# Optimization experiments

Measured on AMD Instinct MI355X. Metric: run time of the kernel, lower is better.

## Reference

```python
import jax, jax.numpy as jnp
import numpy as np

D_MODEL, N_EXPERTS, TOP_K, D_FF = 1024, 8, 2, 4096
B, T = 2, 2048


def setup_inputs() -> dict:
    key = jax.random.key(0)
    k1, k2, k3, k4 = jax.random.split(key, 4)
    x = jax.random.normal(k1, (B, T, D_MODEL), dtype=jnp.float32)
    # kaiming-uniform-ish gate init
    bound = np.sqrt(6.0 / D_MODEL)
    gate_w = jax.random.uniform(k2, (D_MODEL, N_EXPERTS), dtype=jnp.float32, minval=-bound, maxval=bound)
    s1 = 1.0 / np.sqrt(D_MODEL)
    s2 = 1.0 / np.sqrt(D_FF)
    w1 = jax.random.normal(k3, (N_EXPERTS, D_MODEL, D_FF), dtype=jnp.float32) * s1
    w2 = jax.random.normal(k4, (N_EXPERTS, D_FF, D_MODEL), dtype=jnp.float32) * s2
    return {"x": x, "gate_w": gate_w, "w1": w1, "w2": w2}


def reference(x, gate_w, w1, w2):
    Bb, Tt, D = x.shape
    E = w1.shape[0]
    # --- router ---
    logits = jnp.einsum('btd,de->bte', x, gate_w)            # (B,T,E)
    top_v, top_i = jax.lax.top_k(logits, TOP_K)               # (B,T,K)
    weights = jax.nn.softmax(top_v, axis=-1)                  # (B,T,K)
    routing_probs = jax.nn.softmax(logits, axis=-1)           # (B,T,E)
    m = routing_probs.mean(axis=(0, 1))                       # (E,)
    aux_loss = (m * m).sum() * E
    # --- dispatch/combine via dense combine matrix ---
    N = Bb * Tt
    flat_x = x.reshape(N, D)
    idx = top_i.reshape(N, TOP_K)
    w = weights.reshape(N, TOP_K)
    # combine[n,e] = sum_k weights[n,k] * [idx[n,k]==e]
    combine = jnp.zeros((N, E), dtype=x.dtype).at[jnp.arange(N)[:, None], idx].add(w)
    # --- experts: Linear -> GELU(exact) -> Linear (HolographicExpert stand-in) ---
    h = jax.nn.gelu(jnp.einsum('nd,edf->enf', flat_x, w1), approximate=False)  # (E,N,ff)
    y = jnp.einsum('enf,efd->end', h, w2)                                       # (E,N,d)
    out = jnp.einsum('ne,end->nd', combine, y).reshape(Bb, Tt, D)
    return out, aux_loss
```

## Files before the change

### kernel.cpp

```cpp
#include <hip/hip_runtime.h>
#include <hip/hip_bf16.h>

#define DM   1024
#define NE   8
#define DFF  4096
#define NTOK 4096

typedef __attribute__((ext_vector_type(8))) short bf16x8;
typedef __attribute__((ext_vector_type(4))) float f32x4;

__device__ __forceinline__ short to_bf16(float f) {
  unsigned u = __float_as_uint(f);
  unsigned r = (u + 0x7fffu + ((u >> 16) & 1u)) >> 16;
  return (short)r;
}

__device__ __forceinline__ void gl16(const void* g, void* l) {
  __builtin_amdgcn_global_load_lds(
      (const __attribute__((address_space(1))) unsigned*)g,
      (__attribute__((address_space(3))) unsigned*)l, 16, 0, 0);
}

#define DSB do { __builtin_amdgcn_s_barrier(); __builtin_amdgcn_sched_barrier(0); } while (0)

__device__ __forceinline__ float fast_gelu(float v) {
  float x  = fabsf(v) * 0.70710678118f;
  float t  = __builtin_amdgcn_rcpf(fmaf(0.3275911f, x, 1.0f));
  float p  = t * fmaf(t, fmaf(t, fmaf(t, fmaf(t, 1.061405429f, -1.453152027f),
                                      1.421413741f), -0.284496736f), 0.254829592f);
  float ex = __expf(-x * x);
  float er = fmaf(-p, ex, 1.0f);
  er = (v < 0.f) ? -er : er;
  return 0.5f * v * (1.0f + er);
}

__global__ __launch_bounds__(256) void router_kernel(
    const float* __restrict__ x, const float* __restrict__ gw,
    int* __restrict__ cnt, float* __restrict__ psum,
    int* __restrict__ pairs, float* __restrict__ pairW)
{
  __shared__ float gws[DM * NE];
  __shared__ float part[3][64][NE];
  const int tid = threadIdx.x;
  for (int i = tid * 4; i < DM * NE; i += 256 * 4)
    *reinterpret_cast<float4*>(&gws[i]) = *reinterpret_cast<const float4*>(&gw[i]);
  __syncthreads();

  const int tok = tid & 63;
  const int q   = tid >> 6;
  const int n   = blockIdx.x * 64 + tok;
  float acc[NE];
#pragma unroll
  for (int e = 0; e < NE; ++e) acc[e] = 0.f;

  const float4* xr = reinterpret_cast<const float4*>(x + (size_t)n * DM + q * 256);
  for (int d4 = 0; d4 < 64; ++d4) {
    float4 v = xr[d4];
    const float* gp = &gws[(q * 256 + d4 * 4) * NE];
    float xv;
#pragma unroll
    for (int dd = 0; dd < 4; ++dd) {
      xv = (dd == 0) ? v.x : (dd == 1) ? v.y : (dd == 2) ? v.z : v.w;
#pragma unroll
      for (int e = 0; e < NE; ++e) acc[e] = fmaf(xv, gp[dd * NE + e], acc[e]);
    }
  }

  if (q) {
#pragma unroll
    for (int e = 0; e < NE; ++e) part[q - 1][tok][e] = acc[e];
  }
  __syncthreads();
  if (q == 0) {
#pragma unroll
    for (int e = 0; e < NE; ++e)
      acc[e] += part[0][tok][e] + part[1][tok][e] + part[2][tok][e];

    float mx = acc[0];
#pragma unroll
    for (int e = 1; e < NE; ++e) mx = fmaxf(mx, acc[e]);
    float p[NE], s = 0.f;
#pragma unroll
    for (int e = 0; e < NE; ++e) { p[e] = expf(acc[e] - mx); s += p[e]; }
    float inv = 1.f / s;
#pragma unroll
    for (int e = 0; e < NE; ++e) {
      float v = p[e] * inv;
#pragma unroll
      for (int o = 32; o > 0; o >>= 1) v += __shfl_xor(v, o);
      if (tok == 0) atomicAdd(&psum[e], v);
    }

    float v0 = -1e30f, v1 = -1e30f; int i0 = 0, i1 = 0;
#pragma unroll
    for (int e = 0; e < NE; ++e) {
      float l = acc[e];
      if (l > v0) { v1 = v0; i1 = i0; v0 = l; i0 = e; }
      else if (l > v1) { v1 = l; i1 = e; }
    }
    float e1 = expf(v1 - v0);
    float den = 1.f + e1;
    pairW[n * 2]     = 1.f / den;
    pairW[n * 2 + 1] = e1 / den;
    int p0 = atomicAdd(&cnt[i0], 1); pairs[i0 * NTOK + p0] = n * 2;
    int p1 = atomicAdd(&cnt[i1], 1); pairs[i1 * NTOK + p1] = n * 2 + 1;
  }
}

__global__ void finalize_kernel(const int* __restrict__ cnt, int* __restrict__ off,
                                const float* __restrict__ psum, float* __restrict__ aux)
{
  if (threadIdx.x == 0 && blockIdx.x == 0) {
    int o = 0;
    for (int e = 0; e < NE; ++e) { off[e] = o; o += cnt[e]; }
    off[NE] = o;
    float a = 0.f;
    for (int e = 0; e < NE; ++e) { float me = psum[e] * (1.f / NTOK); a += me * me; }
    aux[0] = a * (float)NE;
  }
}

__global__ __launch_bounds__(256) void convert_x_kernel(
    const float* __restrict__ x, short* __restrict__ xb)
{
  const int i = (blockIdx.x * 256 + threadIdx.x) * 8;
  float4 a = *reinterpret_cast<const float4*>(&x[i]);
  float4 b = *reinterpret_cast<const float4*>(&x[i + 4]);
  union { short s[8]; bf16x8 v; } p;
  p.s[0]=to_bf16(a.x); p.s[1]=to_bf16(a.y); p.s[2]=to_bf16(a.z); p.s[3]=to_bf16(a.w);
  p.s[4]=to_bf16(b.x); p.s[5]=to_bf16(b.y); p.s[6]=to_bf16(b.z); p.s[7]=to_bf16(b.w);
  *reinterpret_cast<bf16x8*>(&xb[i]) = p.v;
}

__global__ __launch_bounds__(256) void transpose_kernel(
    const float* __restrict__ w1, const float* __restrict__ w2,
    short* __restrict__ w1t, short* __restrict__ w2t)
{
  const int z = blockIdx.z;
  const float* src; short* dst; int R, C, rt, ct;
  if (z < 8) { src = w1 + (size_t)z * DM * DFF; dst = w1t + (size_t)z * DM * DFF;
               R = DM; C = DFF; ct = blockIdx.x; rt = blockIdx.y; }
  else       { src = w2 + (size_t)(z - 8) * DM * DFF; dst = w2t + (size_t)(z - 8) * DM * DFF;
               R = DFF; C = DM; ct = blockIdx.y; rt = blockIdx.x; }
  const int r0 = rt * 64, c0 = ct * 64;
  __shared__ float t[64][65];
  const int tid = threadIdx.x;
  {
    const int row = tid >> 4;
    const int col = (tid & 15) * 4;
#pragma unroll
    for (int it = 0; it < 4; ++it) {
      float4 v = *reinterpret_cast<const float4*>(&src[(size_t)(r0 + it * 16 + row) * C + c0 + col]);
      t[it * 16 + row][col]     = v.x;
      t[it * 16 + row][col + 1] = v.y;
      t[it * 16 + row][col + 2] = v.z;
      t[it * 16 + row][col + 3] = v.w;
    }
  }
  __syncthreads();
  {
    const int oc  = tid >> 3;
    const int orr = (tid & 7) * 8;
#pragma unroll
    for (int it = 0; it < 2; ++it) {
      union { short s[8]; bf16x8 v; } p;
#pragma unroll
      for (int j = 0; j < 8; ++j) p.s[j] = to_bf16(t[orr + j][it * 32 + oc]);
      *reinterpret_cast<bf16x8*>(&dst[(size_t)(c0 + it * 32 + oc) * R + r0 + orr]) = p.v;
    }
  }
}


#define GEMM_LOOP(NT)                                                              \
  f32x4 acc[4][4];                                                                 \
  _Pragma("unroll") for (int i = 0; i < 4; ++i)                                    \
    _Pragma("unroll") for (int j = 0; j < 4; ++j) acc[i][j] = (f32x4){0.f,0.f,0.f,0.f}; \
  STAGE(0, 0);                                                                     \
  STAGE(1, 32);                                                                    \
  {                                                                                \
    int cur = 0, stg = 2;                                                          \
    for (int t = 0; t < (NT); ++t) {                                               \
      if (t < (NT) - 1) { asm volatile("s_waitcnt vmcnt(4)" ::: "memory"); }       \
      else              { asm volatile("s_waitcnt vmcnt(0)" ::: "memory"); }       \
      DSB;                                                                         \
      if (t + 2 < (NT)) STAGE(stg, (t + 2) * 32);                                  \
      bf16x8 af[4], bfv[4];                                                        \
      _Pragma("unroll") for (int i = 0; i < 4; ++i)                                \
        af[i] = *reinterpret_cast<const bf16x8*>(&As[cur][ab + i * 512]);          \
      _Pragma("unroll") for (int j = 0; j < 4; ++j)                                \
        bfv[j] = *reinterpret_cast<const bf16x8*>(&Bs[cur][bb + j * 512]);         \
      _Pragma("unroll") for (int i = 0; i < 4; ++i)                                \
        _Pragma("unroll") for (int j = 0; j < 4; ++j)                              \
          acc[i][j] = __builtin_amdgcn_mfma_f32_16x16x32_bf16(af[i], bfv[j], acc[i][j], 0, 0, 0); \
      cur = (cur == 2) ? 0 : cur + 1;                                              \
      stg = (stg == 2) ? 0 : stg + 1;                                              \
    }                                                                              \
  }

__global__ __launch_bounds__(256) void gemm1_kernel(
    const short* __restrict__ xb, const short* __restrict__ w1t,
    const int* __restrict__ cnt, const int* __restrict__ off,
    const int* __restrict__ pairs, short* __restrict__ h)
{
  const int wg = (blockIdx.x & 7) * 1024 + (blockIdx.x >> 3);
  const int mt = wg & 31;
  const int ft = (wg >> 5) & 31;
  const int e  = wg >> 10;
  const int M  = cnt[e];
  const int m0 = mt * 128;
  if (m0 >= M) return;
  const int ff0  = ft * 128;
  const int base = off[e];

  __shared__ __attribute__((aligned(16))) short As[3][128 * 32];
  __shared__ __attribute__((aligned(16))) short Bs[3][128 * 32];

  const int tid  = threadIdx.x;
  const int lane = tid & 63;
  const int wv   = tid >> 6;
  const int wm   = wv >> 1;
  const int wn   = wv & 1;

  const short* gA[2]; const short* gB[2]; int ldo[2];
#pragma unroll
  for (int l = 0; l < 2; ++l) {
    const int n   = l * 256 + tid;
    const int p   = n >> 3;
    const int s   = n & 7;
    const int cip = s ^ (p & 7);
    const int row = p * 2 + (cip >> 2);
    const int kch = cip & 3;
    int gi = m0 + row; if (gi > M - 1) gi = M - 1;
    const int tok = pairs[e * NTOK + gi] >> 1;
    gA[l]  = xb + (size_t)tok * DM + kch * 8;
    gB[l]  = w1t + ((size_t)e * DFF + ff0 + row) * DM + kch * 8;
    ldo[l] = n * 8;
  }

#define STAGE(buf, k0) do { \
  gl16(gA[0] + (k0), &As[buf][ldo[0]]); \
  gl16(gA[1] + (k0), &As[buf][ldo[1]]); \
  gl16(gB[0] + (k0), &Bs[buf][ldo[0]]); \
  gl16(gB[1] + (k0), &Bs[buf][ldo[1]]); \
} while (0)

  const int lrw = lane & 15;
  const int sr  = ((((lane & 1) << 2) | (lane >> 4)) ^ ((lane & 15) >> 1)) * 8;
  const int ab  = (wm * 32 + (lrw >> 1)) * 64 + sr;
  const int bb  = (wn * 32 + (lrw >> 1)) * 64 + sr;

  GEMM_LOOP(32)
#undef STAGE

  const int erow0 = m0 + wm * 64 + (lane >> 4) * 4;
  const int ecol0 = ff0 + wn * 64 + (lane & 15);
#pragma unroll
  for (int i = 0; i < 4; ++i) {
#pragma unroll
    for (int r = 0; r < 4; ++r) {
      const int grow = erow0 + i * 16 + r;
      if (grow < M) {
        short* hp = h + (size_t)(base + grow) * DFF + ecol0;
#pragma unroll
        for (int j = 0; j < 4; ++j)
          hp[j * 16] = to_bf16(fast_gelu(acc[i][j][r]));
      }
    }
  }
}

__global__ __launch_bounds__(256) void gemm2_kernel(
    const short* __restrict__ h, const short* __restrict__ w2t,
    const int* __restrict__ cnt, const int* __restrict__ off,
    const int* __restrict__ pairs, const float* __restrict__ pairW,
    float* __restrict__ out)
{
  const int wg = (blockIdx.x & 7) * 256 + (blockIdx.x >> 3);
  const int dt = wg & 7;
  const int mt = (wg >> 3) & 31;
  const int e  = wg >> 8;
  const int M  = cnt[e];
  const int m0 = mt * 128;
  if (m0 >= M) return;
  const int d0   = dt * 128;
  const int base = off[e];

  __shared__ __attribute__((aligned(16))) short As[3][128 * 32];
  __shared__ __attribute__((aligned(16))) short Bs[3][128 * 32];

  const int tid  = threadIdx.x;
  const int lane = tid & 63;
  const int wv   = tid >> 6;
  const int wm   = wv >> 1;
  const int wn   = wv & 1;

  const short* gA[2]; const short* gB[2]; int ldo[2];
#pragma unroll
  for (int l = 0; l < 2; ++l) {
    const int n   = l * 256 + tid;
    const int p   = n >> 3;
    const int s   = n & 7;
    const int cip = s ^ (p & 7);
    const int row = p * 2 + (cip >> 2);
    const int kch = cip & 3;
    int gi = m0 + row; if (gi > M - 1) gi = M - 1;
    gA[l]  = h + (size_t)(base + gi) * DFF + kch * 8;
    gB[l]  = w2t + ((size_t)e * DM + d0 + row) * DFF + kch * 8;
    ldo[l] = n * 8;
  }

#define STAGE(buf, k0) do { \
  gl16(gA[0] + (k0), &As[buf][ldo[0]]); \
  gl16(gA[1] + (k0), &As[buf][ldo[1]]); \
  gl16(gB[0] + (k0), &Bs[buf][ldo[0]]); \
  gl16(gB[1] + (k0), &Bs[buf][ldo[1]]); \
} while (0)

  const int lrw = lane & 15;
  const int sr  = ((((lane & 1) << 2) | (lane >> 4)) ^ ((lane & 15) >> 1)) * 8;
  const int ab  = (wm * 32 + (lrw >> 1)) * 64 + sr;
  const int bb  = (wn * 32 + (lrw >> 1)) * 64 + sr;

  GEMM_LOOP(128)
#undef STAGE

  const int erow0 = m0 + wm * 64 + (lane >> 4) * 4;
  const int ecol0 = d0 + wn * 64 + (lane & 15);
#pragma unroll
  for (int i = 0; i < 4; ++i) {
#pragma unroll
    for (int r = 0; r < 4; ++r) {
      const int grow = erow0 + i * 16 + r;
      if (grow < M) {
        const int pr    = pairs[e * NTOK + grow];
        const float wgt = pairW[pr];
        const int tok   = pr >> 1;
#pragma unroll
        for (int j = 0; j < 4; ++j)
          atomicAdd(&out[(size_t)tok * DM + ecol0 + j * 16], wgt * acc[i][j][r]);
      }
    }
  }
}

extern "C" void kernel_launch(void* const* d_in, const int* in_sizes, int n_in,
                              void* d_out, int out_size, void* d_ws, size_t ws_size,
                              hipStream_t stream)
{
  const float* x  = (const float*)d_in[0];
  const float* gw = (const float*)d_in[1];
  const float* w1 = (const float*)d_in[2];
  const float* w2 = (const float*)d_in[3];
  float* outf = (float*)d_out;

  int*   cnt   = (int*)d_ws;
  int*   off   = cnt + 8;
  float* psum  = (float*)(cnt + 20);
  int*   pairs = (int*)((char*)d_ws + 512);
  float* pairW = (float*)((char*)d_ws + 512 + NE * NTOK * 4);
  short* xb    = (short*)((char*)d_ws + (size_t)(1)  * (1 << 20));
  short* w1t   = (short*)((char*)d_ws + (size_t)(16) * (1 << 20));
  short* w2t   = (short*)((char*)d_ws + (size_t)(80) * (1 << 20));
  short* h     = (short*)((char*)d_ws + (size_t)(144)* (1 << 20));

  hipMemsetAsync(d_ws, 0, 512, stream);
  hipMemsetAsync(d_out, 0, (size_t)out_size * sizeof(float), stream);

  router_kernel<<<NTOK / 64, 256, 0, stream>>>(x, gw, cnt, psum, pairs, pairW);
  finalize_kernel<<<1, 64, 0, stream>>>(cnt, off, psum, outf + (size_t)NTOK * DM);
  convert_x_kernel<<<NTOK * DM / (256 * 8), 256, 0, stream>>>(x, xb);
  transpose_kernel<<<dim3(64, 16, 16), 256, 0, stream>>>(w1, w2, w1t, w2t);
  gemm1_kernel<<<8192, 256, 0, stream>>>(xb, w1t, cnt, off, pairs, h);
  gemm2_kernel<<<2048, 256, 0, stream>>>(h, w2t, cnt, off, pairs, pairW, outf);
}
```

Before: 396.2 us.

## Fuse weight fp32-to-bf16 conversion and transpose into GEMM B-tile loads

```diff
diff --git a/kernel.cpp b/kernel.cpp
--- a/kernel.cpp
+++ b/kernel.cpp
@@ -132,74 +132,74 @@
   *reinterpret_cast<bf16x8*>(&xb[i]) = p.v;
 }
 
-__global__ __launch_bounds__(256) void transpose_kernel(
-    const float* __restrict__ w1, const float* __restrict__ w2,
-    short* __restrict__ w1t, short* __restrict__ w2t)
-{
-  const int z = blockIdx.z;
-  const float* src; short* dst; int R, C, rt, ct;
-  if (z < 8) { src = w1 + (size_t)z * DM * DFF; dst = w1t + (size_t)z * DM * DFF;
-               R = DM; C = DFF; ct = blockIdx.x; rt = blockIdx.y; }
-  else       { src = w2 + (size_t)(z - 8) * DM * DFF; dst = w2t + (size_t)(z - 8) * DM * DFF;
-               R = DFF; C = DM; ct = blockIdx.y; rt = blockIdx.x; }
-  const int r0 = rt * 64, c0 = ct * 64;
-  __shared__ float t[64][65];
-  const int tid = threadIdx.x;
-  {
-    const int row = tid >> 4;
-    const int col = (tid & 15) * 4;
-#pragma unroll
-    for (int it = 0; it < 4; ++it) {
-      float4 v = *reinterpret_cast<const float4*>(&src[(size_t)(r0 + it * 16 + row) * C + c0 + col]);
-      t[it * 16 + row][col]     = v.x;
-      t[it * 16 + row][col + 1] = v.y;
-      t[it * 16 + row][col + 2] = v.z;
-      t[it * 16 + row][col + 3] = v.w;
-    }
-  }
-  __syncthreads();
-  {
-    const int oc  = tid >> 3;
-    const int orr = (tid & 7) * 8;
-#pragma unroll
-    for (int it = 0; it < 2; ++it) {
-      union { short s[8]; bf16x8 v; } p;
-#pragma unroll
-      for (int j = 0; j < 8; ++j) p.s[j] = to_bf16(t[orr + j][it * 32 + oc]);
-      *reinterpret_cast<bf16x8*>(&dst[(size_t)(c0 + it * 32 + oc) * R + r0 + orr]) = p.v;
-    }
-  }
-}
-
-
-#define GEMM_LOOP(NT)                                                              \
+
+#define CVTW(buf, S) do {                                                          \
+    int4 _w0, _w1;                                                                 \
+    asm("v_cvt_pk_bf16_f32 %0, %1, %2" : "=v"(_w0.x) : "v"(S[0].x), "v"(S[1].x)); \
+    asm("v_cvt_pk_bf16_f32 %0, %1, %2" : "=v"(_w0.y) : "v"(S[2].x), "v"(S[3].x)); \
+    asm("v_cvt_pk_bf16_f32 %0, %1, %2" : "=v"(_w0.z) : "v"(S[4].x), "v"(S[5].x)); \
+    asm("v_cvt_pk_bf16_f32 %0, %1, %2" : "=v"(_w0.w) : "v"(S[6].x), "v"(S[7].x)); \
+    asm("v_cvt_pk_bf16_f32 %0, %1, %2" : "=v"(_w1.x) : "v"(S[0].y), "v"(S[1].y)); \
+    asm("v_cvt_pk_bf16_f32 %0, %1, %2" : "=v"(_w1.y) : "v"(S[2].y), "v"(S[3].y)); \
+    asm("v_cvt_pk_bf16_f32 %0, %1, %2" : "=v"(_w1.z) : "v"(S[4].y), "v"(S[5].y)); \
+    asm("v_cvt_pk_bf16_f32 %0, %1, %2" : "=v"(_w1.w) : "v"(S[6].y), "v"(S[7].y)); \
+    *reinterpret_cast<int4*>(&Bs[buf][wo0]) = _w0;                                 \
+    *reinterpret_cast<int4*>(&Bs[buf][wo1]) = _w1;                                 \
+  } while (0)
+
+#define LOADB(S, k0) do {                                                          \
+    const float* _p = gBp + (size_t)(k0) * KSTRIDE;                                \
+    _Pragma("unroll") for (int _j = 0; _j < 8; ++_j)                               \
+      S[_j] = *reinterpret_cast<const float2*>(_p + (size_t)_j * KSTRIDE);         \
+  } while (0)
+
+#define STAGEA(buf, k0) do {                                                       \
+    gl16(gA0 + (k0), &As[buf][ldo0]);                                              \
+    gl16(gA1 + (k0), &As[buf][ldo1]);                                              \
+  } while (0)
+
+#define GITER(t, NT, SC, SL) {                                                     \
+    const int cur = (t) & 1;                                                       \
+    if ((t) < (NT) - 1) { asm volatile("s_waitcnt vmcnt(8)" ::: "memory"); }       \
+    else                { asm volatile("s_waitcnt vmcnt(0)" ::: "memory"); }       \
+    DSB;                                                                           \
+    bf16x8 af[4], bfv[4];                                                          \
+    _Pragma("unroll") for (int _i = 0; _i < 4; ++_i)                               \
+      af[_i] = *reinterpret_cast<const bf16x8*>(&As[cur][ab + _i * 512]);          \
+    _Pragma("unroll") for (int _j = 0; _j < 4; ++_j)                               \
+      bfv[_j] = *reinterpret_cast<const bf16x8*>(&Bs[cur][bb + _j * 512]);         \
+    if ((t) + 1 < (NT)) {                                                          \
+      STAGEA(cur ^ 1, ((t) + 1) * 32);                                             \
+      CVTW(cur ^ 1, SC);                                                           \
+      __builtin_amdgcn_sched_barrier(0);                                           \
+    }                                                                              \
+    if ((t) + 2 < (NT)) LOADB(SL, ((t) + 2) * 32);                                 \
+    _Pragma("unroll") for (int _i = 0; _i < 4; ++_i)                               \
+      _Pragma("unroll") for (int _j = 0; _j < 4; ++_j)                             \
+        acc[_i][_j] = __builtin_amdgcn_mfma_f32_16x16x32_bf16(af[_i], bfv[_j], acc[_i][_j], 0, 0, 0); \
+    asm volatile("s_waitcnt lgkmcnt(0)" ::: "memory");                             \
+  }
+
+#define GEMM_PRO_LOOP(NT)                                                          \
   f32x4 acc[4][4];                                                                 \
   _Pragma("unroll") for (int i = 0; i < 4; ++i)                                    \
     _Pragma("unroll") for (int j = 0; j < 4; ++j) acc[i][j] = (f32x4){0.f,0.f,0.f,0.f}; \
-  STAGE(0, 0);                                                                     \
-  STAGE(1, 32);                                                                    \
-  {                                                                                \
-    int cur = 0, stg = 2;                                                          \
-    for (int t = 0; t < (NT); ++t) {                                               \
-      if (t < (NT) - 1) { asm volatile("s_waitcnt vmcnt(4)" ::: "memory"); }       \
-      else              { asm volatile("s_waitcnt vmcnt(0)" ::: "memory"); }       \
-      DSB;                                                                         \
-      if (t + 2 < (NT)) STAGE(stg, (t + 2) * 32);                                  \
-      bf16x8 af[4], bfv[4];                                                        \
-      _Pragma("unroll") for (int i = 0; i < 4; ++i)                                \
-        af[i] = *reinterpret_cast<const bf16x8*>(&As[cur][ab + i * 512]);          \
-      _Pragma("unroll") for (int j = 0; j < 4; ++j)                                \
-        bfv[j] = *reinterpret_cast<const bf16x8*>(&Bs[cur][bb + j * 512]);         \
-      _Pragma("unroll") for (int i = 0; i < 4; ++i)                                \
-        _Pragma("unroll") for (int j = 0; j < 4; ++j)                              \
-          acc[i][j] = __builtin_amdgcn_mfma_f32_16x16x32_bf16(af[i], bfv[j], acc[i][j], 0, 0, 0); \
-      cur = (cur == 2) ? 0 : cur + 1;                                              \
-      stg = (stg == 2) ? 0 : stg + 1;                                              \
-    }                                                                              \
+  float2 sA[8], sB[8];                                                             \
+  LOADB(sA, 0);                                                                    \
+  __builtin_amdgcn_sched_barrier(0);                                               \
+  STAGEA(0, 0);                                                                    \
+  __builtin_amdgcn_sched_barrier(0);                                               \
+  CVTW(0, sA);                                                                     \
+  __builtin_amdgcn_sched_barrier(0);                                               \
+  LOADB(sA, 32);                                                                   \
+  asm volatile("s_waitcnt lgkmcnt(0)" ::: "memory");                               \
+  for (int t = 0; t < (NT); t += 2) {                                              \
+    GITER(t, (NT), sA, sB)                                                         \
+    GITER(t + 1, (NT), sB, sA)                                                     \
   }
 
 __global__ __launch_bounds__(256) void gemm1_kernel(
-    const short* __restrict__ xb, const short* __restrict__ w1t,
+    const short* __restrict__ xb, const float* __restrict__ w1,
     const int* __restrict__ cnt, const int* __restrict__ off,
     const int* __restrict__ pairs, short* __restrict__ h)
 {
@@ -213,45 +213,40 @@
   const int ff0  = ft * 128;
   const int base = off[e];
 
-  __shared__ __attribute__((aligned(16))) short As[3][128 * 32];
-  __shared__ __attribute__((aligned(16))) short Bs[3][128 * 32];
+  __shared__ __attribute__((aligned(16))) short As[2][4096];
+  __shared__ __attribute__((aligned(16))) short Bs[2][4096];
 
   const int tid  = threadIdx.x;
   const int lane = tid & 63;
   const int wv   = tid >> 6;
-  const int wm   = wv >> 1;
-  const int wn   = wv & 1;
-
-  const short* gA[2]; const short* gB[2]; int ldo[2];
-#pragma unroll
-  for (int l = 0; l < 2; ++l) {
-    const int n   = l * 256 + tid;
-    const int p   = n >> 3;
-    const int s   = n & 7;
-    const int cip = s ^ (p & 7);
-    const int row = p * 2 + (cip >> 2);
-    const int kch = cip & 3;
+  const int wm   = wv >> 1, wn = wv & 1;
+
+  const short *gA0, *gA1; int ldo0, ldo1;
+  {
+    int n = tid, p = n >> 3, s = n & 7, cip = s ^ (p & 7);
+    int row = p * 2 + (cip >> 2), kch = cip & 3;
     int gi = m0 + row; if (gi > M - 1) gi = M - 1;
-    const int tok = pairs[e * NTOK + gi] >> 1;
-    gA[l]  = xb + (size_t)tok * DM + kch * 8;
-    gB[l]  = w1t + ((size_t)e * DFF + ff0 + row) * DM + kch * 8;
-    ldo[l] = n * 8;
-  }
-
-#define STAGE(buf, k0) do { \
-  gl16(gA[0] + (k0), &As[buf][ldo[0]]); \
-  gl16(gA[1] + (k0), &As[buf][ldo[1]]); \
-  gl16(gB[0] + (k0), &Bs[buf][ldo[0]]); \
-  gl16(gB[1] + (k0), &Bs[buf][ldo[1]]); \
-} while (0)
-
-  const int lrw = lane & 15;
-  const int sr  = ((((lane & 1) << 2) | (lane >> 4)) ^ ((lane & 15) >> 1)) * 8;
-  const int ab  = (wm * 32 + (lrw >> 1)) * 64 + sr;
-  const int bb  = (wn * 32 + (lrw >> 1)) * 64 + sr;
-
-  GEMM_LOOP(32)
-#undef STAGE
+    gA0 = xb + (size_t)(pairs[e * NTOK + gi] >> 1) * DM + kch * 8;
+    ldo0 = n * 8;
+    n = 256 + tid; p = n >> 3; s = n & 7; cip = s ^ (p & 7);
+    row = p * 2 + (cip >> 2); kch = cip & 3;
+    gi = m0 + row; if (gi > M - 1) gi = M - 1;
+    gA1 = xb + (size_t)(pairs[e * NTOK + gi] >> 1) * DM + kch * 8;
+    ldo1 = n * 8;
+  }
+
+  const int tkc = tid >> 6;
+  const float* gBp = w1 + (size_t)e * DM * DFF + (size_t)(tkc * 8) * DFF + ff0 + (tid & 63) * 2;
+  const int wo0 = (tid & 63) * 64 + ((tkc) ^ (tid & 7)) * 8;
+  const int wo1 = (tid & 63) * 64 + ((4 | tkc) ^ (tid & 7)) * 8;
+#define KSTRIDE DFF
+
+  const int sr = ((((lane & 1) << 2) | (lane >> 4)) ^ ((lane & 15) >> 1)) * 8;
+  const int ab = (wm * 32 + ((lane & 15) >> 1)) * 64 + sr;
+  const int bb = (wn * 32 + ((lane & 15) >> 1)) * 64 + sr;
+
+  GEMM_PRO_LOOP(32)
+#undef KSTRIDE
 
   const int erow0 = m0 + wm * 64 + (lane >> 4) * 4;
   const int ecol0 = ff0 + wn * 64 + (lane & 15);
@@ -271,7 +266,7 @@
 }
 
 __global__ __launch_bounds__(256) void gemm2_kernel(
-    const short* __restrict__ h, const short* __restrict__ w2t,
+    const short* __restrict__ h, const float* __restrict__ w2,
     const int* __restrict__ cnt, const int* __restrict__ off,
     const int* __restrict__ pairs, const float* __restrict__ pairW,
     float* __restrict__ out)
@@ -286,44 +281,40 @@
   const int d0   = dt * 128;
   const int base = off[e];
 
-  __shared__ __attribute__((aligned(16))) short As[3][128 * 32];
-  __shared__ __attribute__((aligned(16))) short Bs[3][128 * 32];
+  __shared__ __attribute__((aligned(16))) short As[2][4096];
+  __shared__ __attribute__((aligned(16))) short Bs[2][4096];
 
   const int tid  = threadIdx.x;
   const int lane = tid & 63;
   const int wv   = tid >> 6;
-  const int wm   = wv >> 1;
-  const int wn   = wv & 1;
-
-  const short* gA[2]; const short* gB[2]; int ldo[2];
-#pragma unroll
-  for (int l = 0; l < 2; ++l) {
-    const int n   = l * 256 + tid;
-    const int p   = n >> 3;
-    const int s   = n & 7;
-    const int cip = s ^ (p & 7);
-    const int row = p * 2 + (cip >> 2);
-    const int kch = cip & 3;
+  const int wm   = wv >> 1, wn = wv & 1;
+
+  const short *gA0, *gA1; int ldo0, ldo1;
+  {
+    int n = tid, p = n >> 3, s = n & 7, cip = s ^ (p & 7);
+    int row = p * 2 + (cip >> 2), kch = cip & 3;
     int gi = m0 + row; if (gi > M - 1) gi = M - 1;
-    gA[l]  = h + (size_t)(base + gi) * DFF + kch * 8;
-    gB[l]  = w2t + ((size_t)e * DM + d0 + row) * DFF + kch * 8;
-    ldo[l] = n * 8;
-  }
-
-#define STAGE(buf, k0) do { \
-  gl16(gA[0] + (k0), &As[buf][ldo[0]]); \
-  gl16(gA[1] + (k0), &As[buf][ldo[1]]); \
-  gl16(gB[0] + (k0), &Bs[buf][ldo[0]]); \
-  gl16(gB[1] + (k0), &Bs[buf][ldo[1]]); \
-} while (0)
-
-  const int lrw = lane & 15;
-  const int sr  = ((((lane & 1) << 2) | (lane >> 4)) ^ ((lane & 15) >> 1)) * 8;
-  const int ab  = (wm * 32 + (lrw >> 1)) * 64 + sr;
-  const int bb  = (wn * 32 + (lrw >> 1)) * 64 + sr;
-
-  GEMM_LOOP(128)
-#undef STAGE
+    gA0 = h + (size_t)(base + gi) * DFF + kch * 8;
+    ldo0 = n * 8;
+    n = 256 + tid; p = n >> 3; s = n & 7; cip = s ^ (p & 7);
+    row = p * 2 + (cip >> 2); kch = cip & 3;
+    gi = m0 + row; if (gi > M - 1) gi = M - 1;
+    gA1 = h + (size_t)(base + gi) * DFF + kch * 8;
+    ldo1 = n * 8;
+  }
+
+  const int tkc = tid >> 6;
+  const float* gBp = w2 + (size_t)e * DFF * DM + (size_t)(tkc * 8) * DM + d0 + (tid & 63) * 2;
+  const int wo0 = (tid & 63) * 64 + ((tkc) ^ (tid & 7)) * 8;
+  const int wo1 = (tid & 63) * 64 + ((4 | tkc) ^ (tid & 7)) * 8;
+#define KSTRIDE DM
+
+  const int sr = ((((lane & 1) << 2) | (lane >> 4)) ^ ((lane & 15) >> 1)) * 8;
+  const int ab = (wm * 32 + ((lane & 15) >> 1)) * 64 + sr;
+  const int bb = (wn * 32 + ((lane & 15) >> 1)) * 64 + sr;
+
+  GEMM_PRO_LOOP(128)
+#undef KSTRIDE
 
   const int erow0 = m0 + wm * 64 + (lane >> 4) * 4;
   const int ecol0 = d0 + wn * 64 + (lane & 15);
@@ -360,9 +351,7 @@
   int*   pairs = (int*)((char*)d_ws + 512);
   float* pairW = (float*)((char*)d_ws + 512 + NE * NTOK * 4);
   short* xb    = (short*)((char*)d_ws + (size_t)(1)  * (1 << 20));
-  short* w1t   = (short*)((char*)d_ws + (size_t)(16) * (1 << 20));
-  short* w2t   = (short*)((char*)d_ws + (size_t)(80) * (1 << 20));
-  short* h     = (short*)((char*)d_ws + (size_t)(144)* (1 << 20));
+  short* hbuf  = (short*)((char*)d_ws + (size_t)(16) * (1 << 20));
 
   hipMemsetAsync(d_ws, 0, 512, stream);
   hipMemsetAsync(d_out, 0, (size_t)out_size * sizeof(float), stream);
@@ -370,7 +359,6 @@
   router_kernel<<<NTOK / 64, 256, 0, stream>>>(x, gw, cnt, psum, pairs, pairW);
   finalize_kernel<<<1, 64, 0, stream>>>(cnt, off, psum, outf + (size_t)NTOK * DM);
   convert_x_kernel<<<NTOK * DM / (256 * 8), 256, 0, stream>>>(x, xb);
-  transpose_kernel<<<dim3(64, 16, 16), 256, 0, stream>>>(w1, w2, w1t, w2t);
-  gemm1_kernel<<<8192, 256, 0, stream>>>(xb, w1t, cnt, off, pairs, h);
-  gemm2_kernel<<<2048, 256, 0, stream>>>(h, w2t, cnt, off, pairs, pairW, outf);
-}
+  gemm1_kernel<<<8192, 256, 0, stream>>>(xb, w1, cnt, off, pairs, hbuf);
+  gemm2_kernel<<<2048, 256, 0, stream>>>(hbuf, w2, cnt, off, pairs, pairW, outf);
+}
```

Result: slower. 487.4 us (+23.0%).
